# Performance work log

Measured on AMD Instinct MI355X. Metric: run time of the kernel, lower is better.

## Reference

```python
import jax, jax.numpy as jnp
import numpy as np

B, C_IN, C_OUT, H, W = 32, 256, 256, 56, 56
RATE = 0.5
K = int(C_OUT * (1.0 - RATE))  # 128 channels zeroed
BN_EPS = 1e-5


def setup_inputs() -> dict:
    key = jax.random.key(0)
    ks = jax.random.split(key, 4)
    return {
        "x": jax.random.normal(ks[0], (B, C_IN, H, W), dtype=jnp.float32),
        "conv_w": jax.random.normal(ks[1], (C_OUT, C_IN, 3, 3), dtype=jnp.float32) * 0.05,
        "gate_w": jax.random.normal(ks[2], (C_OUT, C_IN), dtype=jnp.float32) * 0.05,
        "gate_b": jnp.ones((C_OUT,), dtype=jnp.float32),
        "bn_gamma": jnp.ones((C_OUT,), dtype=jnp.float32),
        "bn_beta": jnp.zeros((C_OUT,), dtype=jnp.float32),
        "bn_mean": jnp.zeros((C_OUT,), dtype=jnp.float32),
        "bn_var": jnp.ones((C_OUT,), dtype=jnp.float32),
    }


def reference(x, conv_w, gate_w, gate_b, bn_gamma, bn_beta, bn_mean, bn_var):
    # conv2: 3x3, stride 1, padding 1, no bias  -> [B, C_OUT, H, W]
    y = jax.lax.conv_general_dilated(
        x, conv_w, window_strides=(1, 1), padding=((1, 1), (1, 1)),
        dimension_numbers=("NCHW", "OIHW", "NCHW"))
    # BatchNorm2d (eval mode: running stats)
    inv = bn_gamma / jnp.sqrt(bn_var + BN_EPS)
    y = y * inv[None, :, None, None] + (bn_beta - bn_mean * inv)[None, :, None, None]
    # use_relu=True
    y = jax.nn.relu(y)
    # gate: global abs-avg-pool -> linear -> relu   [B, C_OUT]
    s = jnp.mean(jnp.abs(x), axis=(2, 3))  # [B, C_IN]
    g = jax.nn.relu(s @ gate_w.T + gate_b)
    # zero the K smallest gate values per row (topk of -g), then renormalize
    _, idx = jax.lax.top_k(-g, K)  # indices of K smallest
    t = g.at[jnp.arange(B)[:, None], idx].set(0.0)
    t = t / jnp.sum(t, axis=1, keepdims=True) * C_OUT
    # broadcast channel mask
    return y * t[:, :, None, None]
```

## Files before the change

kernel.cpp:

```cpp
#include <hip/hip_runtime.h>
#include <hip/hip_bf16.h>
#include <cstdint>

typedef unsigned short ushort_t;
typedef unsigned int uint_t;
typedef __bf16 bf16x8 __attribute__((ext_vector_type(8)));
typedef float f32x4 __attribute__((ext_vector_type(4)));

#define B_SZ 32
#define C_IN 256
#define C_OUT 256
#define H_SZ 56
#define W_SZ 56
#define HW 3136
#define HP 58
#define WP 58
#define BN_EPS 1e-5f
#define K_ZERO 128

__device__ __forceinline__ ushort_t f2bf(float f) {
    unsigned int u = __builtin_bit_cast(unsigned int, f);
    unsigned int r = (u + 0x7fffu + ((u >> 16) & 1u)) >> 16;
    return (ushort_t)r;
}

__device__ __forceinline__ void load_lds16(const void* gptr, void* ldsptr) {
    __builtin_amdgcn_global_load_lds(
        (const __attribute__((address_space(1))) unsigned int*)(uintptr_t)gptr,
        (__attribute__((address_space(3))) unsigned int*)(uintptr_t)ldsptr,
        16, 0, 0);
}

__global__ __launch_bounds__(256) void prep_w_kernel(const float* __restrict__ w,
                                                     const float* __restrict__ gamma,
                                                     const float* __restrict__ beta,
                                                     const float* __restrict__ mean,
                                                     const float* __restrict__ var,
                                                     ushort_t* __restrict__ Wt,
                                                     float* __restrict__ bninv,
                                                     float* __restrict__ bnadd,
                                                     float* __restrict__ s) {
    int idx = blockIdx.x * 256 + threadIdx.x;
    if (idx < 9 * C_OUT * C_IN) {
        int tap = idx >> 16;
        int rem = idx & 65535;
        int co = rem >> 8, ci = rem & 255;
        Wt[idx] = f2bf(w[(size_t)(co * C_IN + ci) * 9 + tap]);
    }
    if (blockIdx.x < 32) s[idx] = 0.f;
    if (blockIdx.x == 32 && threadIdx.x < C_OUT) {
        int c = threadIdx.x;
        float inv = gamma[c] * rsqrtf(var[c] + BN_EPS);
        bninv[c] = inv;
        bnadd[c] = beta[c] - mean[c] * inv;
    }
}

__global__ __launch_bounds__(256) void prep_x_kernel(const float* __restrict__ x,
                                                     ushort_t* __restrict__ xbp,
                                                     float* __restrict__ s) {
    const int cit = blockIdx.x, h = blockIdx.y, b = blockIdx.z;
    __shared__ float tile[64][57];
    __shared__ float red2[256];
    const int t = threadIdx.x;
    const float* src = x + ((size_t)(b * C_IN + cit * 64) * H_SZ + h) * W_SZ;
    for (int i = t; i < 64 * 14; i += 256) {
        int ci = i / 14, w4 = (i - ci * 14) * 4;
        float4 v = *(const float4*)(src + (size_t)ci * HW + w4);
        tile[ci][w4] = v.x; tile[ci][w4 + 1] = v.y;
        tile[ci][w4 + 2] = v.z; tile[ci][w4 + 3] = v.w;
    }
    __syncthreads();
    {
        int ci = t & 63, wg = t >> 6;
        float a = 0.f;
#pragma unroll
        for (int j = 0; j < 14; j++) a += fabsf(tile[ci][wg * 14 + j]);
        red2[t] = a;
    }
    __syncthreads();
    if (t < 64) {
        float tot = red2[t] + red2[t + 64] + red2[t + 128] + red2[t + 192];
        atomicAdd(&s[b * C_IN + cit * 64 + t], tot * (1.0f / (float)HW));
    }
    const uint2 z2 = make_uint2(0u, 0u);
    for (int i = t; i < W_SZ * 16; i += 256) {
        int w = i >> 4, c4 = (i & 15) * 4;
        uint_t lo = (uint_t)f2bf(tile[c4][w])     | ((uint_t)f2bf(tile[c4 + 1][w]) << 16);
        uint_t hi = (uint_t)f2bf(tile[c4 + 2][w]) | ((uint_t)f2bf(tile[c4 + 3][w]) << 16);
        size_t dst = ((size_t)((b * HP + h + 1) * WP + (w + 1))) * C_IN + cit * 64 + c4;
        *(uint2*)&xbp[dst] = make_uint2(lo, hi);
    }
    if (t < 32) {
        int side = t >> 4, c4 = (t & 15) * 4;
        size_t dst = ((size_t)((b * HP + h + 1) * WP + side * 57)) * C_IN + cit * 64 + c4;
        *(uint2*)&xbp[dst] = z2;
    }
    if (h == 0 || h == 55) {
        int prow = (h == 0) ? 0 : 57;
        for (int i = t; i < 58 * 16; i += 256) {
            int w = i >> 4, c4 = (i & 15) * 4;
            size_t dst = ((size_t)((b * HP + prow) * WP + w)) * C_IN + cit * 64 + c4;
            *(uint2*)&xbp[dst] = z2;
        }
    }
}

__global__ __launch_bounds__(256) void gate_kernel(const float* __restrict__ s,
                                                   const float* __restrict__ gw,
                                                   const float* __restrict__ gb,
                                                   float* __restrict__ tscale) {
    const int b = blockIdx.x, t = threadIdx.x;
    __shared__ float sh_s[C_IN], sh_g[C_OUT], red[256];
    sh_s[t] = s[b * C_IN + t];
    __syncthreads();
    float acc = gb[t];
    const float* wr = gw + (size_t)t * C_IN;
    for (int ci = 0; ci < C_IN; ci++) acc += sh_s[ci] * wr[ci];
    float g = fmaxf(acc, 0.f);
    sh_g[t] = g;
    __syncthreads();
    int cnt = 0;
    for (int j = 0; j < C_OUT; j++) {
        float gj = sh_g[j];
        cnt += (gj < g) || (gj == g && j < t);
    }
    float tv = (cnt >= K_ZERO) ? g : 0.f;
    red[t] = tv;
    __syncthreads();
    for (int off = 128; off > 0; off >>= 1) {
        if (t < off) red[t] += red[t + off];
        __syncthreads();
    }
    tscale[b * C_OUT + t] = tv * ((float)C_OUT / red[0]);
}

__global__ __launch_bounds__(256, 3) void conv_kernel(const ushort_t* __restrict__ xbp,
                                                      const ushort_t* __restrict__ Wt,
                                                      const float* __restrict__ bninv,
                                                      const float* __restrict__ bnadd,
                                                      const float* __restrict__ tscale,
                                                      float* __restrict__ out) {
    __shared__ __align__(16) ushort_t As[128 * 64];
    __shared__ __align__(16) ushort_t Bs[128 * 64];
    const int t = threadIdx.x;
    const int bxr = blockIdx.x;
    const int bx = (bxr >> 4) * 8 + (bxr & 7);
    const int by = (bxr >> 3) & 1;
    const int lane = t & 63;
    const int wv = t >> 6;
    const int waveM = wv >> 1, waveN = wv & 1;

    const int srow = t >> 3;
    const int gxor8 = ((t & 7) ^ (srow & 7)) * 8;
    int arow[4], wrow[4];
#pragma unroll
    for (int i = 0; i < 4; i++) {
        int p = bx * 128 + i * 32 + srow;
        int b = p / HW;
        int r = p - b * HW;
        int hh = r / W_SZ, ww = r - hh * W_SZ;
        arow[i] = ((b * HP + hh + 1) * WP + (ww + 1)) * C_IN + gxor8;
        wrow[i] = (by * 128 + i * 32 + srow) * C_IN + gxor8;
    }
    ushort_t* ldsA = As + t * 8;
    ushort_t* ldsB = Bs + t * 8;

    int aoff[2][4], boff[2][4];
#pragma unroll
    for (int ks = 0; ks < 2; ks++) {
        int c = (lane >> 4) + ks * 4;
#pragma unroll
        for (int mt = 0; mt < 4; mt++) {
            int ra = waveM * 64 + mt * 16 + (lane & 15);
            aoff[ks][mt] = (ra * 8 + (c ^ (ra & 7))) * 16;
            int rb = waveN * 64 + mt * 16 + (lane & 15);
            boff[ks][mt] = (rb * 8 + (c ^ (rb & 7))) * 16;
        }
    }

    f32x4 acc[4][4];
#pragma unroll
    for (int i = 0; i < 4; i++)
#pragma unroll
        for (int j = 0; j < 4; j++) acc[i][j] = (f32x4){0.f, 0.f, 0.f, 0.f};

    const char* Ab = (const char*)As;
    const char* Bb = (const char*)Bs;

    for (int tap = 0; tap < 9; tap++) {
        const int doff = ((tap / 3 - 1) * WP + (tap % 3 - 1)) * C_IN;
        const int woff = tap * (C_OUT * C_IN);
#pragma unroll
        for (int cq = 0; cq < 4; cq++) {
            const int ci0 = cq * 64;
#pragma unroll
            for (int i = 0; i < 4; i++) {
                load_lds16(xbp + arow[i] + doff + ci0, ldsA + i * 2048);
                load_lds16(Wt + wrow[i] + woff + ci0, ldsB + i * 2048);
            }
            __syncthreads();
#pragma unroll
            for (int ks = 0; ks < 2; ks++) {
                bf16x8 af[4], bf[4];
#pragma unroll
                for (int mt = 0; mt < 4; mt++) af[mt] = *(const bf16x8*)(Ab + aoff[ks][mt]);
#pragma unroll
                for (int nt = 0; nt < 4; nt++) bf[nt] = *(const bf16x8*)(Bb + boff[ks][nt]);
#pragma unroll
                for (int mt = 0; mt < 4; mt++)
#pragma unroll
                    for (int nt = 0; nt < 4; nt++)
                        acc[mt][nt] = __builtin_amdgcn_mfma_f32_16x16x32_bf16(
                            af[mt], bf[nt], acc[mt][nt], 0, 0, 0);
            }
            __syncthreads();
        }
    }

#pragma unroll
    for (int mt = 0; mt < 4; mt++) {
        int p0 = bx * 128 + waveM * 64 + mt * 16 + (lane >> 4) * 4;
        int b = p0 / HW;
        int hw = p0 - b * HW;
#pragma unroll
        for (int nt = 0; nt < 4; nt++) {
            int co = by * 128 + waveN * 64 + nt * 16 + (lane & 15);
            float inv = bninv[co], add = bnadd[co], tsc = tscale[b * C_OUT + co];
            float4 o;
            o.x = fmaxf(acc[mt][nt][0] * inv + add, 0.f) * tsc;
            o.y = fmaxf(acc[mt][nt][1] * inv + add, 0.f) * tsc;
            o.z = fmaxf(acc[mt][nt][2] * inv + add, 0.f) * tsc;
            o.w = fmaxf(acc[mt][nt][3] * inv + add, 0.f) * tsc;
            *(float4*)(out + (size_t)(b * C_OUT + co) * HW + hw) = o;
        }
    }
}

extern "C" void kernel_launch(void* const* d_in, const int* in_sizes, int n_in,
                              void* d_out, int out_size, void* d_ws, size_t ws_size,
                              hipStream_t stream) {
    const float* x      = (const float*)d_in[0];
    const float* conv_w = (const float*)d_in[1];
    const float* gate_w = (const float*)d_in[2];
    const float* gate_b = (const float*)d_in[3];
    const float* bn_g   = (const float*)d_in[4];
    const float* bn_b   = (const float*)d_in[5];
    const float* bn_m   = (const float*)d_in[6];
    const float* bn_v   = (const float*)d_in[7];
    float* out = (float*)d_out;

    char* ws = (char*)d_ws;
    float*    s      = (float*)(ws + 0);
    float*    tscale = (float*)(ws + 32768);
    float*    bninv  = (float*)(ws + 65536);
    float*    bnadd  = (float*)(ws + 66560);
    ushort_t* Wt     = (ushort_t*)(ws + 67584);
    ushort_t* xbp    = (ushort_t*)(ws + 1247232);

    prep_w_kernel<<<2304, 256, 0, stream>>>(conv_w, bn_g, bn_b, bn_m, bn_v, Wt, bninv, bnadd, s);
    prep_x_kernel<<<dim3(4, 56, 32), 256, 0, stream>>>(x, xbp, s);
    gate_kernel<<<32, 256, 0, stream>>>(s, gate_w, gate_b, tscale);
    conv_kernel<<<1568, 256, 0, stream>>>(xbp, Wt, bninv, bnadd, tscale, out);
}
```

Baseline: 356.1 us.

## Skip convolution for gated-off channels via per-batch channel permutation

The gate kernel now emits, for each batch, a permutation listing the kept channels first and the zeroed channels after, plus compact scales for the kept ones. The conv kernel is regridded per batch image (25 pixel tiles × 32 batches) and computes only the 128 kept output channels by gathering weight rows through the permutation. It writes zeros for the dropped channels directly. This halves the MFMA work but adds per-image tile padding (3136 is not a multiple of 128), gathered weight loads, and loses the previous L2-friendly block swizzle.

```diff
diff --git a/kernel.cpp b/kernel.cpp
--- a/kernel.cpp
+++ b/kernel.cpp
@@ -109,7 +109,8 @@
 __global__ __launch_bounds__(256) void gate_kernel(const float* __restrict__ s,
                                                    const float* __restrict__ gw,
                                                    const float* __restrict__ gb,
-                                                   float* __restrict__ tscale) {
+                                                   ushort_t* __restrict__ perm,
+                                                   float* __restrict__ cscale) {
     const int b = blockIdx.x, t = threadIdx.x;
     __shared__ float sh_s[C_IN], sh_g[C_OUT], red[256];
     sh_s[t] = s[b * C_IN + t];
@@ -132,21 +133,27 @@
         if (t < off) red[t] += red[t + off];
         __syncthreads();
     }
-    tscale[b * C_OUT + t] = tv * ((float)C_OUT / red[0]);
+    if (cnt >= K_ZERO) {
+        int pos = cnt - K_ZERO;
+        perm[b * C_OUT + pos] = (ushort_t)t;
+        cscale[b * K_ZERO + pos] = tv * ((float)C_OUT / red[0]);
+    } else {
+        perm[b * C_OUT + K_ZERO + cnt] = (ushort_t)t;
+    }
 }
 
 __global__ __launch_bounds__(256, 3) void conv_kernel(const ushort_t* __restrict__ xbp,
                                                       const ushort_t* __restrict__ Wt,
                                                       const float* __restrict__ bninv,
                                                       const float* __restrict__ bnadd,
-                                                      const float* __restrict__ tscale,
+                                                      const ushort_t* __restrict__ perm,
+                                                      const float* __restrict__ cscale,
                                                       float* __restrict__ out) {
     __shared__ __align__(16) ushort_t As[128 * 64];
     __shared__ __align__(16) ushort_t Bs[128 * 64];
     const int t = threadIdx.x;
-    const int bxr = blockIdx.x;
-    const int bx = (bxr >> 4) * 8 + (bxr & 7);
-    const int by = (bxr >> 3) & 1;
+    const int tile = blockIdx.x;
+    const int b = blockIdx.y;
     const int lane = t & 63;
     const int wv = t >> 6;
     const int waveM = wv >> 1, waveN = wv & 1;
@@ -156,12 +163,12 @@
     int arow[4], wrow[4];
 #pragma unroll
     for (int i = 0; i < 4; i++) {
-        int p = bx * 128 + i * 32 + srow;
-        int b = p / HW;
-        int r = p - b * HW;
-        int hh = r / W_SZ, ww = r - hh * W_SZ;
+        int pl = tile * 128 + i * 32 + srow;
+        pl = pl < HW ? pl : HW - 1;
+        int hh = pl / W_SZ, ww = pl - hh * W_SZ;
         arow[i] = ((b * HP + hh + 1) * WP + (ww + 1)) * C_IN + gxor8;
-        wrow[i] = (by * 128 + i * 32 + srow) * C_IN + gxor8;
+        int co = perm[b * C_OUT + i * 32 + srow];
+        wrow[i] = co * C_IN + gxor8;
     }
     ushort_t* ldsA = As + t * 8;
     ushort_t* ldsB = Bs + t * 8;
@@ -218,21 +225,33 @@
         }
     }
 
+    int coK[4], coD[4];
+    float invK[4], addK[4], tscK[4];
+#pragma unroll
+    for (int nt = 0; nt < 4; nt++) {
+        int j = waveN * 64 + nt * 16 + (lane & 15);
+        coK[nt] = perm[b * C_OUT + j];
+        coD[nt] = perm[b * C_OUT + K_ZERO + j];
+        invK[nt] = bninv[coK[nt]];
+        addK[nt] = bnadd[coK[nt]];
+        tscK[nt] = cscale[b * K_ZERO + j];
+    }
+    const float4 z4 = make_float4(0.f, 0.f, 0.f, 0.f);
 #pragma unroll
     for (int mt = 0; mt < 4; mt++) {
-        int p0 = bx * 128 + waveM * 64 + mt * 16 + (lane >> 4) * 4;
-        int b = p0 / HW;
-        int hw = p0 - b * HW;
-#pragma unroll
-        for (int nt = 0; nt < 4; nt++) {
-            int co = by * 128 + waveN * 64 + nt * 16 + (lane & 15);
-            float inv = bninv[co], add = bnadd[co], tsc = tscale[b * C_OUT + co];
-            float4 o;
-            o.x = fmaxf(acc[mt][nt][0] * inv + add, 0.f) * tsc;
-            o.y = fmaxf(acc[mt][nt][1] * inv + add, 0.f) * tsc;
-            o.z = fmaxf(acc[mt][nt][2] * inv + add, 0.f) * tsc;
-            o.w = fmaxf(acc[mt][nt][3] * inv + add, 0.f) * tsc;
-            *(float4*)(out + (size_t)(b * C_OUT + co) * HW + hw) = o;
+        int pl0 = tile * 128 + waveM * 64 + mt * 16 + (lane >> 4) * 4;
+        if (pl0 < HW) {
+#pragma unroll
+            for (int nt = 0; nt < 4; nt++) {
+                float inv = invK[nt], add = addK[nt], tsc = tscK[nt];
+                float4 o;
+                o.x = fmaxf(acc[mt][nt][0] * inv + add, 0.f) * tsc;
+                o.y = fmaxf(acc[mt][nt][1] * inv + add, 0.f) * tsc;
+                o.z = fmaxf(acc[mt][nt][2] * inv + add, 0.f) * tsc;
+                o.w = fmaxf(acc[mt][nt][3] * inv + add, 0.f) * tsc;
+                *(float4*)(out + (size_t)(b * C_OUT + coK[nt]) * HW + pl0) = o;
+                *(float4*)(out + (size_t)(b * C_OUT + coD[nt]) * HW + pl0) = z4;
+            }
         }
     }
 }
@@ -252,7 +271,8 @@
 
     char* ws = (char*)d_ws;
     float*    s      = (float*)(ws + 0);
-    float*    tscale = (float*)(ws + 32768);
+    ushort_t* perm   = (ushort_t*)(ws + 32768);
+    float*    cscale = (float*)(ws + 49152);
     float*    bninv  = (float*)(ws + 65536);
     float*    bnadd  = (float*)(ws + 66560);
     ushort_t* Wt     = (ushort_t*)(ws + 67584);
@@ -260,6 +280,6 @@
 
     prep_w_kernel<<<2304, 256, 0, stream>>>(conv_w, bn_g, bn_b, bn_m, bn_v, Wt, bninv, bnadd, s);
     prep_x_kernel<<<dim3(4, 56, 32), 256, 0, stream>>>(x, xbp, s);
-    gate_kernel<<<32, 256, 0, stream>>>(s, gate_w, gate_b, tscale);
-    conv_kernel<<<1568, 256, 0, stream>>>(xbp, Wt, bninv, bnadd, tscale, out);
-}
+    gate_kernel<<<32, 256, 0, stream>>>(s, gate_w, gate_b, perm, cscale);
+    conv_kernel<<<dim3(25, 32), 256, 0, stream>>>(xbp, Wt, bninv, bnadd, perm, cscale, out);
+}
```

New measurement: 327.4 us. -8.1%, faster.
